# Kernel optimization log

Measured on AMD Instinct MI355X. Metric: run time of the kernel, lower is better.

The kernel has to match this reference:

```python
import jax, jax.numpy as jnp
import numpy as np

EPS = 1e-5
NUM_CLASSES = 8

def _conv(x, w, b):
    # reflect pad 1 then valid 3x3 conv, NCHW / OIHW
    x = jnp.pad(x, ((0, 0), (0, 0), (1, 1), (1, 1)), mode='reflect')
    y = jax.lax.conv_general_dilated(x, w, (1, 1), 'VALID',
        dimension_numbers=('NCHW', 'OIHW', 'NCHW'))
    return y + b[None, :, None, None]

def _up2(x):
    B, C, H, W = x.shape
    return jax.image.resize(x, (B, C, 2 * H, 2 * W), method='bilinear')

def _nearest_resize_seg(seg, H, W):
    # torch F.interpolate mode='nearest': src = floor(dst * in / out)
    ih = jnp.arange(H) * seg.shape[2] // H
    iw = jnp.arange(W) * seg.shape[3] // W
    return seg[:, :, ih][:, :, :, iw]

def _seg_norm(x, seg):
    # per-class InstanceNorm2d (no affine) on masked copies, summed
    H, W = x.shape[2], x.shape[3]
    seg_r = _nearest_resize_seg(seg, H, W)  # [B,1,H,W]
    out = jnp.zeros_like(x)
    for c in range(NUM_CLASSES):
        mask = (seg_r == c).astype(x.dtype)
        xc = x * mask
        mu = jnp.mean(xc, axis=(2, 3), keepdims=True)
        var = jnp.mean(xc * xc, axis=(2, 3), keepdims=True) - mu * mu
        out = out + (xc - mu) * jax.lax.rsqrt(var + EPS)
    return out

def setup_inputs() -> dict:
    key = jax.random.key(0)
    ks = jax.random.split(key, 24)
    d = {}
    d['x'] = jax.random.normal(ks[0], (4, 512, 64, 64), dtype=jnp.float32)
    d['seg_map'] = jax.random.randint(ks[1], (4, 1, 64, 64), 0, NUM_CLASSES, dtype=jnp.int32)
    shapes = [(256, 512), (256, 256), (256, 256), (256, 256), (128, 256),
              (128, 128), (64, 128), (64, 64), (3, 64)]
    names = ['1', '2', '3', '4', '5', '6', '7', '8', 'f']
    for i, ((o, ic), nm) in enumerate(zip(shapes, names)):
        fan_in = ic * 9
        bound = 1.0 / np.sqrt(fan_in)
        d['w' + nm] = jax.random.uniform(ks[2 + 2 * i], (o, ic, 3, 3), jnp.float32, -bound, bound)
        d['b' + nm] = jax.random.uniform(ks[3 + 2 * i], (o,), jnp.float32, -bound, bound)
    return d

def reference(x, seg_map, w1, b1, w2, b2, w3, b3, w4, b4, w5, b5,
              w6, b6, w7, b7, w8, b8, wf, bf):
    h = jax.nn.relu(_conv(x, w1, b1))
    h = _seg_norm(h, seg_map)
    h = _up2(h)
    h = jax.nn.relu(_conv(h, w2, b2))
    h = jax.nn.relu(_conv(h, w3, b3))
    h = jax.nn.relu(_conv(h, w4, b4))
    h = jax.nn.relu(_conv(h, w5, b5))
    h = _seg_norm(h, seg_map)
    h = _up2(h)
    h = jax.nn.relu(_conv(h, w6, b6))
    h = jax.nn.relu(_conv(h, w7, b7))
    h = _seg_norm(h, seg_map)
    h = _up2(h)
    h = jax.nn.relu(_conv(h, w8, b8))
    return _conv(h, wf, bf)
```

## Files before the change

kernel.cpp:

```cpp
#include <hip/hip_runtime.h>

typedef unsigned int uint;
typedef unsigned short ushort;
typedef __bf16 bf16x8 __attribute__((ext_vector_type(8)));
typedef float f32x4 __attribute__((ext_vector_type(4)));
typedef uint u32x4 __attribute__((ext_vector_type(4)));
typedef ushort u16x4 __attribute__((ext_vector_type(4)));

__device__ __forceinline__ float bf_lo(uint u) { return __builtin_bit_cast(float, u << 16); }
__device__ __forceinline__ float bf_hi(uint u) { return __builtin_bit_cast(float, u & 0xFFFF0000u); }
__device__ __forceinline__ ushort f2bf(float f) {
  uint u = __builtin_bit_cast(uint, f);
  return (ushort)((u + 0x7FFFu + ((u >> 16) & 1u)) >> 16);
}

template<int NCH, int ROWS, int II, int RELU>
__global__ __launch_bounds__(256) void conv_mfma_k(
    const ushort* __restrict__ in, const ushort* __restrict__ wp,
    const float* __restrict__ bias, ushort* __restrict__ out,
    int Cout, int H, int W,
    int in_row0, int in_rows, int out_row0, int out_rows,
    int ob_row0, int ob_rows) {
  constexpr int Cin = NCH * 32;
  constexpr int COB = II * 16;
  constexpr int SLOTS = (ROWS + 2) * 66 * 4;
  constexpr int NPASS = (SLOTS + 255) / 256;
  constexpr int LAST = SLOTS - (NPASS - 1) * 256;
  __shared__ ushort lds[2][SLOTS * 8];
  const int tid = threadIdx.x;
  const int lane = tid & 63;
  const int wv = tid >> 6;
  const int wx0 = blockIdx.x * 64;
  const int nCoB = Cout / COB;
  const int cob = (blockIdx.z % nCoB) * COB;
  const int b = blockIdx.z / nCoB;
  const int h0 = out_row0 + blockIdx.y * ROWS;
  const int nCb = Cout >> 4;
  const int cb0 = cob >> 4;

  int hs[ROWS + 2];
#pragma unroll
  for (int r = 0; r < ROWS + 2; ++r) {
    int hh = h0 - 1 + r;
    if (hh < 0) hh = 1;
    if (hh >= H) hh = 2 * (H - 1) - hh;
    hh = min(max(hh, in_row0), in_row0 + in_rows - 1);
    hs[r] = hh - in_row0;
  }

  const ushort* gsrc[NPASS];
  uint lof[NPASS];
#pragma unroll
  for (int p = 0; p < NPASS; ++p) {
    const int t = p * 256 + tid;
    const int px_g = t >> 2, kgs = t & 3;
    int rr = px_g / 66;
    int px = px_g - rr * 66;
    if (rr > ROWS + 1) { px = px_g - (ROWS + 2) * 66; rr = ROWS + 1; }
    const int kg = kgs ^ ((px >> 1) & 3);
    int wsrc = wx0 + px - 1;
    wsrc = (wsrc < 0) ? 1 : (wsrc >= W ? W - 2 : wsrc);
    gsrc[p] = in + ((size_t)(b * in_rows + hs[rr]) * W + wsrc) * Cin + kg * 8;
    lof[p] = (uint)((p * 256 + wv * 64) * 8);
  }

  const int bpx = wv * 16 + (lane & 15);
  const int bkg = lane >> 4;

  f32x4 acc[ROWS][II] = {};

  auto stage = [&](int buf, int ci0) {
#pragma unroll
    for (int p = 0; p < NPASS; ++p) {
      if (p + 1 < NPASS || tid < LAST)
        __builtin_amdgcn_global_load_lds(
            (const __attribute__((address_space(1))) void*)(gsrc[p] + ci0),
            (__attribute__((address_space(3))) void*)(&lds[buf][lof[p]]), 16, 0, 0);
    }
  };
  auto compute = [&](int buf, int kc) {
    const ushort* lb = &lds[buf][0];
#pragma unroll
    for (int t9 = 0; t9 < 9; ++t9) {
      const int dr = t9 / 3, s = t9 - dr * 3;
      bf16x8 afr[II];
#pragma unroll
      for (int ii = 0; ii < II; ++ii) {
        const int off = (((t9 * nCb + cb0 + ii) * NCH + kc) << 9) + (lane << 3);
        afr[ii] = __builtin_bit_cast(bf16x8, *(const u32x4*)(wp + off));
      }
      const int px = bpx + s;
      const int swz = bkg ^ ((px >> 1) & 3);
#pragma unroll
      for (int rr = 0; rr < ROWS; ++rr) {
        const int sl = (((rr + dr) * 66 + px) << 2) + swz;
        const bf16x8 bfrag = __builtin_bit_cast(bf16x8, *(const u32x4*)(lb + sl * 8));
#pragma unroll
        for (int ii = 0; ii < II; ++ii)
          acc[rr][ii] = __builtin_amdgcn_mfma_f32_16x16x32_bf16(afr[ii], bfrag, acc[rr][ii], 0, 0, 0);
      }
    }
  };

  stage(0, 0);
  asm volatile("s_waitcnt vmcnt(0)" ::: "memory");
  __syncthreads();
#pragma unroll 1
  for (int c = 0; c < NCH; ++c) {
    if (c + 1 < NCH) stage((c + 1) & 1, (c + 1) * 32);
    compute(c & 1, c);
    asm volatile("s_waitcnt vmcnt(0)" ::: "memory");
    __syncthreads();
  }

  const int cofr = cob + (lane >> 4) * 4;
  const int pxo = wx0 + bpx;
#pragma unroll
  for (int rr = 0; rr < ROWS; ++rr) {
    const int h = h0 + rr;
    if (h >= out_row0 + out_rows) break;
    const size_t base = ((size_t)(b * ob_rows + (h - ob_row0)) * W + pxo) * Cout;
#pragma unroll
    for (int ii = 0; ii < II; ++ii) {
      u16x4 pk;
#pragma unroll
      for (int g = 0; g < 4; ++g) {
        float v = acc[rr][ii][g] + bias[cofr + ii * 16 + g];
        if (RELU) v = fmaxf(v, 0.f);
        pk[g] = f2bf(v);
      }
      *(u16x4*)(out + base + cofr + ii * 16) = pk;
    }
  }
}

__global__ __launch_bounds__(256) void convf_mfma_k(
    const ushort* __restrict__ in, const ushort* __restrict__ wp,
    const float* __restrict__ bias, float* __restrict__ out,
    int in_row0, int in_rows, int out_row0, int out_rows) {
  constexpr int ROWS = 4, NCH = 2, W = 512, H = 512, Cin = 64;
  constexpr int SLOTS = (ROWS + 2) * 66 * 4;
  constexpr int NPASS = (SLOTS + 255) / 256;
  constexpr int LAST = SLOTS - (NPASS - 1) * 256;
  __shared__ ushort lds[2][SLOTS * 8];
  const int tid = threadIdx.x;
  const int lane = tid & 63;
  const int wv = tid >> 6;
  const int wx0 = blockIdx.x * 64;
  const int b = blockIdx.z;
  const int h0 = out_row0 + blockIdx.y * ROWS;

  int hs[ROWS + 2];
#pragma unroll
  for (int r = 0; r < ROWS + 2; ++r) {
    int hh = h0 - 1 + r;
    if (hh < 0) hh = 1;
    if (hh >= H) hh = 2 * (H - 1) - hh;
    hh = min(max(hh, in_row0), in_row0 + in_rows - 1);
    hs[r] = hh - in_row0;
  }
  const ushort* gsrc[NPASS];
  uint lof[NPASS];
#pragma unroll
  for (int p = 0; p < NPASS; ++p) {
    const int t = p * 256 + tid;
    const int px_g = t >> 2, kgs = t & 3;
    int rr = px_g / 66;
    int px = px_g - rr * 66;
    if (rr > ROWS + 1) { px = px_g - (ROWS + 2) * 66; rr = ROWS + 1; }
    const int kg = kgs ^ ((px >> 1) & 3);
    int wsrc = wx0 + px - 1;
    wsrc = (wsrc < 0) ? 1 : (wsrc >= W ? W - 2 : wsrc);
    gsrc[p] = in + ((size_t)(b * in_rows + hs[rr]) * W + wsrc) * Cin + kg * 8;
    lof[p] = (uint)((p * 256 + wv * 64) * 8);
  }
  const int bpx = wv * 16 + (lane & 15);
  const int bkg = lane >> 4;
  f32x4 acc[ROWS] = {};

  auto stage = [&](int buf, int ci0) {
#pragma unroll
    for (int p = 0; p < NPASS; ++p) {
      if (p + 1 < NPASS || tid < LAST)
        __builtin_amdgcn_global_load_lds(
            (const __attribute__((address_space(1))) void*)(gsrc[p] + ci0),
            (__attribute__((address_space(3))) void*)(&lds[buf][lof[p]]), 16, 0, 0);
    }
  };
  auto compute = [&](int buf, int kc) {
    const ushort* lb = &lds[buf][0];
#pragma unroll
    for (int t9 = 0; t9 < 9; ++t9) {
      const int dr = t9 / 3, s = t9 - dr * 3;
      const int off = (((t9 * NCH) + kc) << 9) + (lane << 3);
      const bf16x8 afr = __builtin_bit_cast(bf16x8, *(const u32x4*)(wp + off));
      const int px = bpx + s;
      const int swz = bkg ^ ((px >> 1) & 3);
#pragma unroll
      for (int rr = 0; rr < ROWS; ++rr) {
        const int sl = (((rr + dr) * 66 + px) << 2) + swz;
        const bf16x8 bfrag = __builtin_bit_cast(bf16x8, *(const u32x4*)(lb + sl * 8));
        acc[rr] = __builtin_amdgcn_mfma_f32_16x16x32_bf16(afr, bfrag, acc[rr], 0, 0, 0);
      }
    }
  };

  stage(0, 0);
  asm volatile("s_waitcnt vmcnt(0)" ::: "memory");
  __syncthreads();
#pragma unroll 1
  for (int c = 0; c < NCH; ++c) {
    if (c + 1 < NCH) stage((c + 1) & 1, (c + 1) * 32);
    compute(c & 1, c);
    asm volatile("s_waitcnt vmcnt(0)" ::: "memory");
    __syncthreads();
  }

  if ((lane >> 4) == 0) {
    const int pxo = wx0 + bpx;
#pragma unroll
    for (int rr = 0; rr < ROWS; ++rr) {
      const int h = h0 + rr;
      if (h >= out_row0 + out_rows) break;
#pragma unroll
      for (int g = 0; g < 3; ++g)
        out[(((size_t)(b * 3 + g)) << 18) + ((size_t)h << 9) + pxo] = acc[rr][g] + bias[g];
    }
  }
}

__global__ __launch_bounds__(256) void sn_sum_k(
    const ushort* __restrict__ x, const int* __restrict__ seg,
    float* __restrict__ Ssum, float* __restrict__ Qsum, int C, int logW, int nsl) {
  const int W = 1 << logW, sh = logW - 6;
  const int b = blockIdx.x / nsl, sl = blockIdx.x % nsl;
  const int PPT = 256 / C;
  const int c = threadIdx.x % C;
  const int sub = threadIdx.x / C;
  const int rows = W / nsl;
  const int p0 = sl * rows * W;
  const int np = rows * W;
  const ushort* xp = x + ((size_t)b << (2 * logW)) * C + (size_t)p0 * C;
  const int* segb = seg + (b << 12);
  float S[8] = {0, 0, 0, 0, 0, 0, 0, 0};
  float Q[8] = {0, 0, 0, 0, 0, 0, 0, 0};
  for (int k = sub; k < np; k += PPT) {
    const int p = p0 + k;
    const int cls = segb[(((p >> logW) >> sh) << 6) + ((p & (W - 1)) >> sh)];
    const uint u = xp[(size_t)k * C + c];
    const float v = __builtin_bit_cast(float, u << 16);
#pragma unroll
    for (int t = 0; t < 8; ++t) {
      const bool m = (cls == t);
      S[t] += m ? v : 0.f;
      Q[t] += m ? v * v : 0.f;
    }
  }
#pragma unroll
  for (int t = 0; t < 8; ++t) {
    atomicAdd(&Ssum[((b << 3) + t) * C + c], S[t]);
    atomicAdd(&Qsum[((b << 3) + t) * C + c], Q[t]);
  }
}

__global__ void sn_fin_k(const float* __restrict__ Ssum, const float* __restrict__ Qsum,
                         float* __restrict__ RS, float* __restrict__ KK, int C, float invN) {
  const int tid = threadIdx.x;
  const int b = tid / C, c = tid % C;
  float K = 0.f;
#pragma unroll
  for (int t = 0; t < 8; ++t) {
    const float s = Ssum[((b << 3) + t) * C + c];
    const float q = Qsum[((b << 3) + t) * C + c];
    const float mu = s * invN;
    const float var = q * invN - mu * mu;
    const float r = rsqrtf(var + 1e-5f);
    RS[((b << 3) + t) * C + c] = r;
    K += mu * r;
  }
  KK[b * C + c] = K;
}

__global__ __launch_bounds__(256) void up2norm_k(
    const ushort* __restrict__ src, const int* __restrict__ seg,
    const float* __restrict__ RS, const float* __restrict__ KK,
    ushort* __restrict__ out, int C, int logWs, int out_row0, int out_rows) {
  const int Ws = 1 << logWs, W2 = Ws << 1, sh = logWs - 6;
  const int cpb = C >> 3;
  int i = blockIdx.x * 256 + threadIdx.x;
  const int total = 4 * out_rows * W2 * cpb;
  if (i >= total) return;
  const int cc = (i % cpb) * 8; i /= cpb;
  const int ow = i % W2; i /= W2;
  const int r = i % out_rows;
  const int b = i / out_rows;
  const int oh = out_row0 + r;

  int hl = (oh - 1) >> 1;
  const float hf = (oh & 1) ? 0.25f : 0.75f;
  const int hh = min(hl + 1, Ws - 1);
  hl = max(hl, 0);
  int wl = (ow - 1) >> 1;
  const float wfc = (ow & 1) ? 0.25f : 0.75f;
  const int wh = min(wl + 1, Ws - 1);
  wl = max(wl, 0);

  const size_t pl = (size_t)b << (2 * logWs);
  const u32x4 xll = *(const u32x4*)(src + ((pl + hl * Ws + wl) * C + cc));
  const u32x4 xlh = *(const u32x4*)(src + ((pl + hl * Ws + wh) * C + cc));
  const u32x4 xhl = *(const u32x4*)(src + ((pl + hh * Ws + wl) * C + cc));
  const u32x4 xhh = *(const u32x4*)(src + ((pl + hh * Ws + wh) * C + cc));
  const int* segb = seg + (b << 12);
  const int cll = segb[((hl >> sh) << 6) + (wl >> sh)];
  const int clh = segb[((hl >> sh) << 6) + (wh >> sh)];
  const int chl = segb[((hh >> sh) << 6) + (wl >> sh)];
  const int chh = segb[((hh >> sh) << 6) + (wh >> sh)];
  const float* rll = RS + ((b << 3) + cll) * C + cc;
  const float* rlh = RS + ((b << 3) + clh) * C + cc;
  const float* rhl = RS + ((b << 3) + chl) * C + cc;
  const float* rhh = RS + ((b << 3) + chh) * C + cc;
  const float* kk = KK + b * C + cc;

  u32x4 res;
#pragma unroll
  for (int q = 0; q < 4; ++q) {
    const int c0 = 2 * q, c1 = 2 * q + 1;
    const float na0 = bf_lo(xll[q]) * rll[c0], nb0 = bf_lo(xlh[q]) * rlh[c0];
    const float nc0 = bf_lo(xhl[q]) * rhl[c0], nd0 = bf_lo(xhh[q]) * rhh[c0];
    const float na1 = bf_hi(xll[q]) * rll[c1], nb1 = bf_hi(xlh[q]) * rlh[c1];
    const float nc1 = bf_hi(xhl[q]) * rhl[c1], nd1 = bf_hi(xhh[q]) * rhh[c1];
    const float t0 = na0 + wfc * (nb0 - na0), bo0 = nc0 + wfc * (nd0 - nc0);
    const float t1 = na1 + wfc * (nb1 - na1), bo1 = nc1 + wfc * (nd1 - nc1);
    const float o0 = t0 + hf * (bo0 - t0) - kk[c0];
    const float o1 = t1 + hf * (bo1 - t1) - kk[c1];
    res[q] = (uint)f2bf(o0) | ((uint)f2bf(o1) << 16);
  }
  *(u32x4*)(out + (((size_t)(b * out_rows + r)) * W2 + ow) * C + cc) = res;
}

struct PWSeg { const float* w; ushort* p; int Co, Ci; };
struct PackArgs { PWSeg s[8]; };
__global__ __launch_bounds__(256) void packall_k(PackArgs a) {
  int i = blockIdx.x * 256 + threadIdx.x;
#pragma unroll
  for (int k = 0; k < 8; ++k) {
    const int Co = a.s[k].Co, Ci = a.s[k].Ci;
    const int tot = Co * Ci * 9;
    if (i < tot) {
      const int nKc = Ci >> 5, nCb = Co >> 4;
      const int j = i & 7, l = (i >> 3) & 63;
      int rest = i >> 9;
      const int kc = rest % nKc; rest /= nKc;
      const int cb = rest % nCb;
      const int t9 = rest / nCb;
      const int co = cb * 16 + (l & 15);
      const int ci = kc * 32 + (l >> 4) * 8 + j;
      a.s[k].p[i] = f2bf(a.s[k].w[((size_t)(co * Ci + ci)) * 9 + t9]);
      return;
    }
    i -= tot;
  }
}

__global__ __launch_bounds__(256) void packwf_k(const float* __restrict__ w,
                                                ushort* __restrict__ wp) {
  const int i = blockIdx.x * 256 + threadIdx.x;
  if (i >= 9216) return;
  const int j = i & 7;
  const int l = (i >> 3) & 63;
  const int rest = i >> 9;
  const int kc = rest & 1;
  const int t9 = rest >> 1;
  const int co = l & 15;
  const int ci = kc * 32 + (l >> 4) * 8 + j;
  wp[i] = (co < 3) ? f2bf(w[((size_t)(co * 64 + ci)) * 9 + t9]) : (ushort)0;
}

__global__ __launch_bounds__(256) void cvt_x_k(const float* __restrict__ x,
                                               ushort* __restrict__ xn) {
  __shared__ float tile[32][65];
  const int p0 = blockIdx.x * 64, c0 = blockIdx.y * 32, b = blockIdx.z;
  for (int k = threadIdx.x; k < 2048; k += 256) {
    const int ci = k >> 6, pj = k & 63;
    tile[ci][pj] = x[(((size_t)(b * 512 + c0 + ci)) << 12) + p0 + pj];
  }
  __syncthreads();
  for (int k = threadIdx.x; k < 2048; k += 256) {
    const int ci = k & 31, pj = k >> 5;
    xn[((((size_t)b << 12) + p0 + pj)) * 512 + c0 + ci] = f2bf(tile[ci][pj]);
  }
}

extern "C" void kernel_launch(void* const* d_in, const int* in_sizes, int n_in,
                              void* d_out, int out_size, void* d_ws, size_t ws_size,
                              hipStream_t stream) {
  const float* x = (const float*)d_in[0];
  const int* seg = (const int*)d_in[1];
  const float *w1 = (const float*)d_in[2], *b1 = (const float*)d_in[3];
  const float *w2 = (const float*)d_in[4], *b2 = (const float*)d_in[5];
  const float *w3 = (const float*)d_in[6], *b3 = (const float*)d_in[7];
  const float *w4 = (const float*)d_in[8], *b4 = (const float*)d_in[9];
  const float *w5 = (const float*)d_in[10], *b5 = (const float*)d_in[11];
  const float *w6 = (const float*)d_in[12], *b6 = (const float*)d_in[13];
  const float *w7 = (const float*)d_in[14], *b7 = (const float*)d_in[15];
  const float *w8 = (const float*)d_in[16], *b8 = (const float*)d_in[17];
  const float *wf = (const float*)d_in[18], *bf = (const float*)d_in[19];
  float* outp = (float*)d_out;

  char* wsb = (char*)d_ws;
  const size_t MB = 1048576;
  ushort* w1p = (ushort*)(wsb + 0);
  ushort* w2p = (ushort*)(wsb + 2359296);
  ushort* w3p = (ushort*)(wsb + 3538944);
  ushort* w4p = (ushort*)(wsb + 4718592);
  ushort* w5p = (ushort*)(wsb + 5898240);
  ushort* w6p = (ushort*)(wsb + 6488064);
  ushort* w7p = (ushort*)(wsb + 6782976);
  ushort* w8p = (ushort*)(wsb + 6930432);
  ushort* wfp = (ushort*)(wsb + 7004160);
  float* Ssum = (float*)(wsb + 8388608);
  float* Qsum = (float*)(wsb + 8421376);
  float* RS = (float*)(wsb + 8454144);
  float* KK = (float*)(wsb + 8486912);
  ushort* XN = (ushort*)(wsb + 9 * MB);
  ushort* A1 = (ushort*)(wsb + 25 * MB);
  ushort* U1 = (ushort*)(wsb + 33 * MB);
  ushort* C2 = (ushort*)(wsb + 65 * MB);
  ushort* C3 = (ushort*)(wsb + 9 * MB);
  ushort* C4 = (ushort*)(wsb + 41 * MB);
  ushort* C5 = (ushort*)(wsb + 9 * MB);
  ushort* U6 = (ushort*)(wsb + 25 * MB);
  ushort* C6 = (ushort*)(wsb + 58 * MB);
  ushort* C7 = (ushort*)(wsb + 91 * MB);
  ushort* U8 = (ushort*)(wsb + 9 * MB);
  ushort* C8 = (ushort*)(wsb + 43 * MB);

  auto cdiv = [](int a, int b) { return (a + b - 1) / b; };

  cvt_x_k<<<dim3(64, 16, 4), 256, 0, stream>>>(x, XN);
  PackArgs pa;
  pa.s[0] = {w1, w1p, 256, 512};
  pa.s[1] = {w2, w2p, 256, 256};
  pa.s[2] = {w3, w3p, 256, 256};
  pa.s[3] = {w4, w4p, 256, 256};
  pa.s[4] = {w5, w5p, 128, 256};
  pa.s[5] = {w6, w6p, 128, 128};
  pa.s[6] = {w7, w7p, 64, 128};
  pa.s[7] = {w8, w8p, 64, 64};
  packall_k<<<cdiv(3502080, 256), 256, 0, stream>>>(pa);
  packwf_k<<<36, 256, 0, stream>>>(wf, wfp);

  conv_mfma_k<16, 2, 8, 1><<<dim3(1, 32, 8), 256, 0, stream>>>(
      XN, w1p, b1, A1, 256, 64, 64, 0, 64, 0, 64, 0, 64);
  hipMemsetAsync(Ssum, 0, 65536, stream);
  sn_sum_k<<<4 * 32, 256, 0, stream>>>(A1, seg, Ssum, Qsum, 256, 6, 32);
  sn_fin_k<<<1, 1024, 0, stream>>>(Ssum, Qsum, RS, KK, 256, 1.f / 4096.f);
  up2norm_k<<<cdiv(4 * 128 * 128 * 32, 256), 256, 0, stream>>>(A1, seg, RS, KK, U1, 256, 6, 0, 128);

  conv_mfma_k<8, 4, 8, 1><<<dim3(2, 32, 8), 256, 0, stream>>>(
      U1, w2p, b2, C2, 256, 128, 128, 0, 128, 0, 128, 0, 128);
  conv_mfma_k<8, 4, 8, 1><<<dim3(2, 32, 8), 256, 0, stream>>>(
      C2, w3p, b3, C3, 256, 128, 128, 0, 128, 0, 128, 0, 128);
  conv_mfma_k<8, 4, 8, 1><<<dim3(2, 32, 8), 256, 0, stream>>>(
      C3, w4p, b4, C4, 256, 128, 128, 0, 128, 0, 128, 0, 128);
  conv_mfma_k<8, 4, 8, 1><<<dim3(2, 32, 4), 256, 0, stream>>>(
      C4, w5p, b5, C5, 128, 128, 128, 0, 128, 0, 128, 0, 128);
  hipMemsetAsync(Ssum, 0, 65536, stream);
  sn_sum_k<<<4 * 64, 256, 0, stream>>>(C5, seg, Ssum, Qsum, 128, 7, 64);
  sn_fin_k<<<1, 512, 0, stream>>>(Ssum, Qsum, RS, KK, 128, 1.f / 16384.f);

  for (int kb = 0; kb < 2; ++kb) {
    const int r0 = kb * 128;
    const int Rlo = max(r0 - 1, 0), Rhi = min(r0 + 128, 255);
    const int rows6 = Rhi - Rlo + 1;
    const int Ulo = max(Rlo - 1, 0), Uhi = min(Rhi + 1, 255);
    const int rowsU = Uhi - Ulo + 1;
    up2norm_k<<<cdiv(4 * rowsU * 256 * 16, 256), 256, 0, stream>>>(C5, seg, RS, KK, U6, 128, 7, Ulo, rowsU);
    conv_mfma_k<4, 4, 8, 1><<<dim3(4, cdiv(rows6, 4), 4), 256, 0, stream>>>(
        U6, w6p, b6, C6, 128, 256, 256, Ulo, rowsU, Rlo, rows6, Rlo, rows6);
    conv_mfma_k<4, 4, 4, 1><<<dim3(4, 32, 4), 256, 0, stream>>>(
        C6, w7p, b7, C7, 64, 256, 256, Rlo, rows6, r0, 128, 0, 256);
  }
  hipMemsetAsync(Ssum, 0, 65536, stream);
  sn_sum_k<<<4 * 128, 256, 0, stream>>>(C7, seg, Ssum, Qsum, 64, 8, 128);
  sn_fin_k<<<1, 256, 0, stream>>>(Ssum, Qsum, RS, KK, 64, 1.f / 65536.f);

  for (int kb = 0; kb < 4; ++kb) {
    const int r0 = kb * 128;
    const int Rlo = max(r0 - 1, 0), Rhi = min(r0 + 128, 511);
    const int rows8 = Rhi - Rlo + 1;
    const int Ulo = max(Rlo - 1, 0), Uhi = min(Rhi + 1, 511);
    const int rowsU = Uhi - Ulo + 1;
    up2norm_k<<<cdiv(4 * rowsU * 512 * 8, 256), 256, 0, stream>>>(C7, seg, RS, KK, U8, 64, 8, Ulo, rowsU);
    conv_mfma_k<2, 4, 4, 1><<<dim3(8, cdiv(rows8, 4), 4), 256, 0, stream>>>(
        U8, w8p, b8, C8, 64, 512, 512, Ulo, rowsU, Rlo, rows8, Rlo, rows8);
    convf_mfma_k<<<dim3(8, 32, 4), 256, 0, stream>>>(C8, wfp, bf, outp, Rlo, rows8, r0, 128);
  }
}
```

Baseline: 1.409 ms.

## Split conv work across waves by output channel instead of pixel

```diff
diff --git a/kernel.cpp b/kernel.cpp
--- a/kernel.cpp
+++ b/kernel.cpp
@@ -14,7 +14,7 @@
   return (ushort)((u + 0x7FFFu + ((u >> 16) & 1u)) >> 16);
 }
 
-template<int NCH, int ROWS, int II, int RELU>
+template<int NCH, int ROWS, int RELU>
 __global__ __launch_bounds__(256) void conv_mfma_k(
     const ushort* __restrict__ in, const ushort* __restrict__ wp,
     const float* __restrict__ bias, ushort* __restrict__ out,
@@ -22,21 +22,21 @@
     int in_row0, int in_rows, int out_row0, int out_rows,
     int ob_row0, int ob_rows) {
   constexpr int Cin = NCH * 32;
-  constexpr int COB = II * 16;
   constexpr int SLOTS = (ROWS + 2) * 66 * 4;
   constexpr int NPASS = (SLOTS + 255) / 256;
   constexpr int LAST = SLOTS - (NPASS - 1) * 256;
+  constexpr int ROWBYTES = 66 * 4 * 16;
   __shared__ ushort lds[2][SLOTS * 8];
   const int tid = threadIdx.x;
   const int lane = tid & 63;
   const int wv = tid >> 6;
   const int wx0 = blockIdx.x * 64;
-  const int nCoB = Cout / COB;
-  const int cob = (blockIdx.z % nCoB) * COB;
+  const int nCoB = Cout >> 6;
+  const int cob = (blockIdx.z % nCoB) * 64;
   const int b = blockIdx.z / nCoB;
   const int h0 = out_row0 + blockIdx.y * ROWS;
   const int nCb = Cout >> 4;
-  const int cb0 = cob >> 4;
+  const int cb0 = (cob >> 4) + wv;
 
   int hs[ROWS + 2];
 #pragma unroll
@@ -64,10 +64,17 @@
     lof[p] = (uint)((p * 256 + wv * 64) * 8);
   }
 
-  const int bpx = wv * 16 + (lane & 15);
-  const int bkg = lane >> 4;
-
-  f32x4 acc[ROWS][II] = {};
+  uint boff[4][3];
+#pragma unroll
+  for (int g = 0; g < 4; ++g)
+#pragma unroll
+    for (int s = 0; s < 3; ++s) {
+      const int px = g * 16 + (lane & 15) + s;
+      const uint swz = (uint)((lane >> 4) ^ ((px >> 1) & 3));
+      boff[g][s] = (uint)((px * 4 + swz) * 16);
+    }
+
+  f32x4 acc[4][ROWS] = {};
 
   auto stage = [&](int buf, int ci0) {
 #pragma unroll
@@ -79,25 +86,20 @@
     }
   };
   auto compute = [&](int buf, int kc) {
-    const ushort* lb = &lds[buf][0];
+    const char* lb = (const char*)(&lds[buf][0]);
 #pragma unroll
     for (int t9 = 0; t9 < 9; ++t9) {
       const int dr = t9 / 3, s = t9 - dr * 3;
-      bf16x8 afr[II];
-#pragma unroll
-      for (int ii = 0; ii < II; ++ii) {
-        const int off = (((t9 * nCb + cb0 + ii) * NCH + kc) << 9) + (lane << 3);
-        afr[ii] = __builtin_bit_cast(bf16x8, *(const u32x4*)(wp + off));
-      }
-      const int px = bpx + s;
-      const int swz = bkg ^ ((px >> 1) & 3);
-#pragma unroll
-      for (int rr = 0; rr < ROWS; ++rr) {
-        const int sl = (((rr + dr) * 66 + px) << 2) + swz;
-        const bf16x8 bfrag = __builtin_bit_cast(bf16x8, *(const u32x4*)(lb + sl * 8));
-#pragma unroll
-        for (int ii = 0; ii < II; ++ii)
-          acc[rr][ii] = __builtin_amdgcn_mfma_f32_16x16x32_bf16(afr[ii], bfrag, acc[rr][ii], 0, 0, 0);
+      const int aoff = (((t9 * nCb + cb0) * NCH + kc) << 9) + (lane << 3);
+      const bf16x8 afr = __builtin_bit_cast(bf16x8, *(const u32x4*)(wp + aoff));
+#pragma unroll
+      for (int g = 0; g < 4; ++g) {
+#pragma unroll
+        for (int rr = 0; rr < ROWS; ++rr) {
+          const bf16x8 bfrag = __builtin_bit_cast(
+              bf16x8, *(const u32x4*)(lb + boff[g][s] + (rr + dr) * ROWBYTES));
+          acc[g][rr] = __builtin_amdgcn_mfma_f32_16x16x32_bf16(afr, bfrag, acc[g][rr], 0, 0, 0);
+        }
       }
     }
   };
@@ -113,23 +115,23 @@
     __syncthreads();
   }
 
-  const int cofr = cob + (lane >> 4) * 4;
-  const int pxo = wx0 + bpx;
+  const int cofr = cob + wv * 16 + (lane >> 4) * 4;
 #pragma unroll
   for (int rr = 0; rr < ROWS; ++rr) {
     const int h = h0 + rr;
     if (h >= out_row0 + out_rows) break;
-    const size_t base = ((size_t)(b * ob_rows + (h - ob_row0)) * W + pxo) * Cout;
-#pragma unroll
-    for (int ii = 0; ii < II; ++ii) {
+    const size_t rowbase = (size_t)(b * ob_rows + (h - ob_row0)) * W;
+#pragma unroll
+    for (int g = 0; g < 4; ++g) {
+      const int pxo = wx0 + g * 16 + (lane & 15);
       u16x4 pk;
 #pragma unroll
-      for (int g = 0; g < 4; ++g) {
-        float v = acc[rr][ii][g] + bias[cofr + ii * 16 + g];
+      for (int j = 0; j < 4; ++j) {
+        float v = acc[g][rr][j] + bias[cofr + j];
         if (RELU) v = fmaxf(v, 0.f);
-        pk[g] = f2bf(v);
+        pk[j] = f2bf(v);
       }
-      *(u16x4*)(out + base + cofr + ii * 16) = pk;
+      *(u16x4*)(out + (rowbase + pxo) * Cout + cofr) = pk;
     }
   }
 }
@@ -450,20 +452,20 @@
   packall_k<<<cdiv(3502080, 256), 256, 0, stream>>>(pa);
   packwf_k<<<36, 256, 0, stream>>>(wf, wfp);
 
-  conv_mfma_k<16, 2, 8, 1><<<dim3(1, 32, 8), 256, 0, stream>>>(
+  conv_mfma_k<16, 2, 1><<<dim3(1, 32, 16), 256, 0, stream>>>(
       XN, w1p, b1, A1, 256, 64, 64, 0, 64, 0, 64, 0, 64);
   hipMemsetAsync(Ssum, 0, 65536, stream);
   sn_sum_k<<<4 * 32, 256, 0, stream>>>(A1, seg, Ssum, Qsum, 256, 6, 32);
   sn_fin_k<<<1, 1024, 0, stream>>>(Ssum, Qsum, RS, KK, 256, 1.f / 4096.f);
   up2norm_k<<<cdiv(4 * 128 * 128 * 32, 256), 256, 0, stream>>>(A1, seg, RS, KK, U1, 256, 6, 0, 128);
 
-  conv_mfma_k<8, 4, 8, 1><<<dim3(2, 32, 8), 256, 0, stream>>>(
+  conv_mfma_k<8, 4, 1><<<dim3(2, 32, 16), 256, 0, stream>>>(
       U1, w2p, b2, C2, 256, 128, 128, 0, 128, 0, 128, 0, 128);
-  conv_mfma_k<8, 4, 8, 1><<<dim3(2, 32, 8), 256, 0, stream>>>(
+  conv_mfma_k<8, 4, 1><<<dim3(2, 32, 16), 256, 0, stream>>>(
       C2, w3p, b3, C3, 256, 128, 128, 0, 128, 0, 128, 0, 128);
-  conv_mfma_k<8, 4, 8, 1><<<dim3(2, 32, 8), 256, 0, stream>>>(
+  conv_mfma_k<8, 4, 1><<<dim3(2, 32, 16), 256, 0, stream>>>(
       C3, w4p, b4, C4, 256, 128, 128, 0, 128, 0, 128, 0, 128);
-  conv_mfma_k<8, 4, 8, 1><<<dim3(2, 32, 4), 256, 0, stream>>>(
+  conv_mfma_k<8, 4, 1><<<dim3(2, 32, 8), 256, 0, stream>>>(
       C4, w5p, b5, C5, 128, 128, 128, 0, 128, 0, 128, 0, 128);
   hipMemsetAsync(Ssum, 0, 65536, stream);
   sn_sum_k<<<4 * 64, 256, 0, stream>>>(C5, seg, Ssum, Qsum, 128, 7, 64);
@@ -476,9 +478,9 @@
     const int Ulo = max(Rlo - 1, 0), Uhi = min(Rhi + 1, 255);
     const int rowsU = Uhi - Ulo + 1;
     up2norm_k<<<cdiv(4 * rowsU * 256 * 16, 256), 256, 0, stream>>>(C5, seg, RS, KK, U6, 128, 7, Ulo, rowsU);
-    conv_mfma_k<4, 4, 8, 1><<<dim3(4, cdiv(rows6, 4), 4), 256, 0, stream>>>(
+    conv_mfma_k<4, 4, 1><<<dim3(4, cdiv(rows6, 4), 8), 256, 0, stream>>>(
         U6, w6p, b6, C6, 128, 256, 256, Ulo, rowsU, Rlo, rows6, Rlo, rows6);
-    conv_mfma_k<4, 4, 4, 1><<<dim3(4, 32, 4), 256, 0, stream>>>(
+    conv_mfma_k<4, 4, 1><<<dim3(4, 32, 4), 256, 0, stream>>>(
         C6, w7p, b7, C7, 64, 256, 256, Rlo, rows6, r0, 128, 0, 256);
   }
   hipMemsetAsync(Ssum, 0, 65536, stream);
@@ -492,7 +494,7 @@
     const int Ulo = max(Rlo - 1, 0), Uhi = min(Rhi + 1, 511);
     const int rowsU = Uhi - Ulo + 1;
     up2norm_k<<<cdiv(4 * rowsU * 512 * 8, 256), 256, 0, stream>>>(C7, seg, RS, KK, U8, 64, 8, Ulo, rowsU);
-    conv_mfma_k<2, 4, 4, 1><<<dim3(8, cdiv(rows8, 4), 4), 256, 0, stream>>>(
+    conv_mfma_k<2, 4, 1><<<dim3(8, cdiv(rows8, 4), 4), 256, 0, stream>>>(
         U8, w8p, b8, C8, 64, 512, 512, Ulo, rowsU, Rlo, rows8, Rlo, rows8);
     convf_mfma_k<<<dim3(8, 32, 4), 256, 0, stream>>>(C8, wfp, bf, outp, Rlo, rows8, r0, 128);
   }
```

Result: slower. 1.458 ms (+3.5%).
